# Optimization experiments

Hardware: AMD Instinct MI355X
Metric: run time of the kernel (lower is better)

## Reference

```python
import jax, jax.numpy as jnp
import numpy as np

B, N, D, H, DG = 1, 1024, 512, 8, 64
DK = D // H
EPS = 1e-5


def _layer_norm(x, g, b):
    m = jnp.mean(x, axis=-1, keepdims=True)
    v = jnp.var(x, axis=-1, keepdims=True)
    return (x - m) / jnp.sqrt(v + EPS) * g + b


def _box_rel_embedding(box):
    # box: (B, N, 4) = x_min, y_min, x_max, y_max
    x_min, y_min, x_max, y_max = [box[..., i] for i in range(4)]  # each (B, N)
    cx = (x_min + x_max) * 0.5
    cy = (y_min + y_max) * 0.5
    w = x_max - x_min + 1.0
    h = y_max - y_min + 1.0
    dx = jnp.log(jnp.clip(jnp.abs((cx[:, :, None] - cx[:, None, :]) / w[:, :, None]), 0.001))
    dy = jnp.log(jnp.clip(jnp.abs((cy[:, :, None] - cy[:, None, :]) / h[:, :, None]), 0.001))
    dw = jnp.log(w[:, :, None] / w[:, None, :])
    dh = jnp.log(h[:, :, None] / h[:, None, :])
    pos = jnp.stack([dx, dy, dw, dh], axis=-1)  # (B, N, N, 4)
    dim_mat = 1.0 / jnp.power(1000.0, jnp.arange(DG // 8, dtype=jnp.float32) / (DG // 8))  # (8,)
    mul = (100.0 * pos[..., None] * dim_mat).reshape(pos.shape[0], pos.shape[1], pos.shape[2], -1)  # (B,N,N,32)
    return jnp.concatenate([jnp.sin(mul), jnp.cos(mul)], axis=-1)  # (B, N, N, 64)


def _split_heads(x, W, b):
    # torch permute(2,0,1,3).view(-1, len, d_k): head-major flattening
    return (x @ W.T + b).reshape(B, N, H, DK).transpose(2, 0, 1, 3).reshape(H * B, N, DK)


def _forward(input_query, input_key, input_value, input_box,
             Wq, bq, Wk, bk, Wv, bv, Wo, bo, WG_w, WG_b,
             ln0_g, ln0_b, ln_g, ln_b):
    residual = input_query
    emb = _box_rel_embedding(input_box)  # (B, N, N, 64)
    # per-head linear (64 -> 1) then relu: (B, H, N, N)
    w_g = jax.nn.relu(jnp.einsum('bijg,hg->bhij', emb, WG_w) + WG_b[None, :, None, None])
    q = _split_heads(input_query, Wq, bq)  # (H*B, N, DK)
    k = _split_heads(input_key, Wk, bk)
    v = _split_heads(input_value, Wv, bv)
    scores = jnp.einsum('xnd,xmd->xnm', q, k) / np.sqrt(DK).astype(np.float32)  # (H*B, N, N)
    # original adds (B,H,N,N) to (H*B,N,N): only valid for B==1
    w_mn = jax.nn.softmax(jnp.log(jnp.clip(w_g.reshape(H * B, N, N), 1e-6)) + scores, axis=-1)
    x = jnp.einsum('xnm,xmd->xnd', w_mn, v)  # (H*B, N, DK)
    # faithful to original: transpose(1,2) then view(nbatches, -1, h*d_k)
    x = x.transpose(0, 2, 1).reshape(B, -1, H * DK)  # (B, N, D)
    out0 = _layer_norm(x + residual, ln0_g, ln0_b)
    out = out0 @ Wo.T + bo  # dropout = identity (eval mode)
    return _layer_norm(out + out0, ln_g, ln_b)


def setup_inputs() -> dict:
    key = jax.random.key(0)
    ks = jax.random.split(key, 12)
    inp = {}
    inp['input_query'] = jax.random.normal(ks[0], (B, N, D), dtype=jnp.float32)
    inp['input_key'] = jax.random.normal(ks[1], (B, N, D), dtype=jnp.float32)
    inp['input_value'] = jax.random.normal(ks[2], (B, N, D), dtype=jnp.float32)
    mins = jax.random.uniform(ks[3], (B, N, 2), dtype=jnp.float32) * 500.0
    sizes = jax.random.uniform(ks[4], (B, N, 2), dtype=jnp.float32) * 99.0 + 1.0
    inp['input_box'] = jnp.concatenate([mins, mins + sizes], axis=-1)  # valid boxes
    s = 0.02
    inp['Wq'] = jax.random.normal(ks[5], (D, D), dtype=jnp.float32) * s
    inp['bq'] = jnp.zeros((D,), dtype=jnp.float32)
    inp['Wk'] = jax.random.normal(ks[6], (D, D), dtype=jnp.float32) * s
    inp['bk'] = jnp.zeros((D,), dtype=jnp.float32)
    inp['Wv'] = jax.random.normal(ks[7], (D, D), dtype=jnp.float32) * s
    inp['bv'] = jnp.zeros((D,), dtype=jnp.float32)
    inp['Wo'] = jax.random.normal(ks[8], (D, D), dtype=jnp.float32) * s
    inp['bo'] = jnp.zeros((D,), dtype=jnp.float32)
    inp['WG_w'] = jax.random.normal(ks[9], (H, DG), dtype=jnp.float32) * 0.1
    inp['WG_b'] = jax.random.normal(ks[10], (H,), dtype=jnp.float32) * 0.1
    inp['ln0_g'] = jnp.ones((D,), dtype=jnp.float32)
    inp['ln0_b'] = jnp.zeros((D,), dtype=jnp.float32)
    inp['ln_g'] = jnp.ones((D,), dtype=jnp.float32)
    inp['ln_b'] = jnp.zeros((D,), dtype=jnp.float32)
    return inp


def reference(input_query, input_key, input_value, input_box,
              Wq, bq, Wk, bk, Wv, bv, Wo, bo, WG_w, WG_b,
              ln0_g, ln0_b, ln_g, ln_b):
    return _forward(input_query, input_key, input_value, input_box,
                    Wq, bq, Wk, bk, Wv, bv, Wo, bo, WG_w, WG_b,
                    ln0_g, ln0_b, ln_g, ln_b)
```

## Files before the change

kernel.cpp:

```cpp
#include <hip/hip_runtime.h>
#include <cstddef>

#define NTOK 1024
#define DMODEL 512
#define NHEAD 8
#define DKH 64
#define NSPLIT 4
#define JQ 256

typedef __attribute__((ext_vector_type(4))) float f32x4;
typedef __attribute__((ext_vector_type(8))) __bf16 bf16x8;
typedef __attribute__((ext_vector_type(4))) __bf16 bf16x4;
typedef __attribute__((ext_vector_type(4))) unsigned short u16x4;
typedef __attribute__((ext_vector_type(8))) unsigned short u16x8;
typedef __attribute__((ext_vector_type(4))) _Float16 f16x4;
typedef unsigned short ushort_t;

__device__ __forceinline__ float wave_sum_f(float v){
  #pragma unroll
  for (int m=1; m<64; m<<=1) v += __shfl_xor(v, m, 64);
  return v;
}
__device__ __forceinline__ unsigned short f2bf(float f){
  __bf16 b = (__bf16)f;
  return __builtin_bit_cast(unsigned short, b);
}
__device__ __forceinline__ float bf2f(unsigned short u){
  return (float)__builtin_bit_cast(__bf16, u);
}

__device__ __forceinline__ float fract_hw(float x){
  float r; asm("v_fract_f32 %0, %1" : "=v"(r) : "v"(x)); return r;
}
__device__ __forceinline__ float sin_rev(float rev){
  float f = fract_hw(rev);
  float s; asm("v_sin_f32 %0, %1" : "=v"(s) : "v"(f)); return s;
}
__device__ __forceinline__ float cos_rev(float rev){
  float f = fract_hw(rev);
  float c; asm("v_cos_f32 %0, %1" : "=v"(c) : "v"(f)); return c;
}
__device__ __forceinline__ float log_hw(float x){
  float l; asm("v_log_f32 %0, %1" : "=v"(l) : "v"(x));
  return 0.69314718056f * l;
}
__device__ __forceinline__ float exp_hw(float x){
  float y = x * 1.44269504f;
  float e; asm("v_exp_f32 %0, %1" : "=v"(e) : "v"(y));
  return e;
}

__global__ __launch_bounds__(256) void k_front2(
    const float* __restrict__ box, const float* __restrict__ WGw, const float* __restrict__ WGb,
    _Float16* __restrict__ wg16,
    const float* __restrict__ inq, const float* __restrict__ ink, const float* __restrict__ inv,
    const float* __restrict__ Wq, const float* __restrict__ Wk, const float* __restrict__ Wv,
    const float* __restrict__ Wo,
    const float* __restrict__ bq, const float* __restrict__ bk, const float* __restrict__ bv,
    ushort_t* __restrict__ Qb, ushort_t* __restrict__ Kb, ushort_t* __restrict__ Vt,
    ushort_t* __restrict__ Wob){
  __shared__ __align__(16) char smem[17408];
  const int t = threadIdx.x;
  const int lane = t & 63, w = t >> 6, li = lane & 15, g = lane >> 4;
  if (blockIdx.x >= 1408){
    int off = ((blockIdx.x - 1408)*256 + t)*8;
    float4 a = *(const float4*)(Wo + off);
    float4 b4 = *(const float4*)(Wo + off + 4);
    u16x4 o0, o1;
    o0[0]=f2bf(a.x); o0[1]=f2bf(a.y); o0[2]=f2bf(a.z); o0[3]=f2bf(a.w);
    o1[0]=f2bf(b4.x); o1[1]=f2bf(b4.y); o1[2]=f2bf(b4.z); o1[3]=f2bf(b4.w);
    *(u16x4*)(Wob + off) = o0;
    *(u16x4*)(Wob + off + 4) = o1;
    return;
  }
  if (blockIdx.x >= 1024){
    const int u = blockIdx.x - 1024;
    const int z = u >> 7;
    const int rem = u & 127;
    const int m0 = (rem >> 3)*64;
    const int n0 = (rem & 7)*64;
    const float* A = z==0 ? inq : z==1 ? ink : inv;
    const float* W = z==0 ? Wq : z==1 ? Wk : Wv;
    const float* bias = z==0 ? bq : z==1 ? bk : bv;
    ushort_t* Al = (ushort_t*)smem;
    ushort_t* Wl = (ushort_t*)(smem + 8704);
    const int row = t >> 2, kq = (t & 3)*16;
    const int mrb = (w >> 1)*32;
    const int nrb = (w & 1)*32;
    f32x4 acc[2][2] = {};
    for (int k0 = 0; k0 < DMODEL; k0 += 64){
      {
        const float* ap = A + (size_t)(m0+row)*DMODEL + k0 + kq;
        const float* wp = W + (size_t)(n0+row)*DMODEL + k0 + kq;
        #pragma unroll
        for (int q=0; q<4; q++){
          float4 av = *(const float4*)(ap + q*4);
          float4 wv = *(const float4*)(wp + q*4);
          u16x4 pa, pw;
          pa[0]=f2bf(av.x); pa[1]=f2bf(av.y); pa[2]=f2bf(av.z); pa[3]=f2bf(av.w);
          pw[0]=f2bf(wv.x); pw[1]=f2bf(wv.y); pw[2]=f2bf(wv.z); pw[3]=f2bf(wv.w);
          *(u16x4*)(Al + row*68 + kq + q*4) = pa;
          *(u16x4*)(Wl + row*68 + kq + q*4) = pw;
        }
      }
      __syncthreads();
      #pragma unroll
      for (int kc=0; kc<64; kc+=32){
        const ushort_t* arl = Al + (mrb + li)*68 + kc + g*8;
        const ushort_t* wrl = Wl + (nrb + li)*68 + kc + g*8;
        bf16x8 af0 = *(const bf16x8*)(arl);
        bf16x8 af1 = *(const bf16x8*)(arl + 16*68);
        bf16x8 wf0 = *(const bf16x8*)(wrl);
        bf16x8 wf1 = *(const bf16x8*)(wrl + 16*68);
        if (z < 2){
          acc[0][0] = __builtin_amdgcn_mfma_f32_16x16x32_bf16(wf0, af0, acc[0][0], 0,0,0);
          acc[0][1] = __builtin_amdgcn_mfma_f32_16x16x32_bf16(wf0, af1, acc[0][1], 0,0,0);
          acc[1][0] = __builtin_amdgcn_mfma_f32_16x16x32_bf16(wf1, af0, acc[1][0], 0,0,0);
          acc[1][1] = __builtin_amdgcn_mfma_f32_16x16x32_bf16(wf1, af1, acc[1][1], 0,0,0);
        } else {
          acc[0][0] = __builtin_amdgcn_mfma_f32_16x16x32_bf16(af0, wf0, acc[0][0], 0,0,0);
          acc[0][1] = __builtin_amdgcn_mfma_f32_16x16x32_bf16(af0, wf1, acc[0][1], 0,0,0);
          acc[1][0] = __builtin_amdgcn_mfma_f32_16x16x32_bf16(af1, wf0, acc[1][0], 0,0,0);
          acc[1][1] = __builtin_amdgcn_mfma_f32_16x16x32_bf16(af1, wf1, acc[1][1], 0,0,0);
        }
      }
      __syncthreads();
    }
    if (z < 2){
      ushort_t* C = z ? Kb : Qb;
      #pragma unroll
      for (int nf=0; nf<2; nf++){
        int n = n0 + nrb + nf*16 + g*4;
        float4 b4 = *(const float4*)(bias + n);
        const float* bp = (const float*)&b4;
        #pragma unroll
        for (int mf=0; mf<2; mf++){
          int m = m0 + mrb + mf*16 + li;
          u16x4 o;
          #pragma unroll
          for (int r=0; r<4; r++) o[r] = f2bf(acc[nf][mf][r] + bp[r]);
          *(u16x4*)(C + (size_t)m*DMODEL + n) = o;
        }
      }
    } else {
      #pragma unroll
      for (int mf=0; mf<2; mf++){
        int m = m0 + mrb + mf*16 + g*4;
        #pragma unroll
        for (int nf=0; nf<2; nf++){
          int n = n0 + nrb + nf*16 + li;
          float bn = bias[n];
          u16x4 o;
          #pragma unroll
          for (int r=0; r<4; r++) o[r] = f2bf(acc[mf][nf][r] + bn);
          *(u16x4*)(Vt + (((size_t)(n>>6))<<16) + ((size_t)(n&63)<<10) + m) = o;
        }
      }
    }
    return;
  }
  float* arr = (float*)smem;
  #pragma unroll
  for (int u2=0; u2<4; u2++){
    int idx = u2*256 + t;
    float4 b4 = *(const float4*)(box + idx*4);
    arr[idx]        = (b4.x + b4.z)*0.5f;
    arr[1024+idx]   = (b4.y + b4.w)*0.5f;
    arr[2048+idx]   = log_hw(b4.z - b4.x + 1.0f);
    arr[3072+idx]   = log_hw(b4.w - b4.y + 1.0f);
  }
  const int i = blockIdx.x;
  float4 bi = *(const float4*)(box + i*4);
  float wi = bi.z - bi.x + 1.0f, hi = bi.w - bi.y + 1.0f;
  float Pi = (g==0) ? (bi.x+bi.z)*0.5f : (g==1) ? (bi.y+bi.w)*0.5f
           : (g==2) ? log_hw(wi) : log_hw(hi);
  float Ri = (g==0) ? 1.0f/wi : (g==1) ? 1.0f/hi : 1.0f;
  const bool doLog = (g < 2);
  bf16x8 wfs = {}, wfc = {};
  float wgb_li = 0.0f;
  if (li < 8){
    #pragma unroll
    for (int e=0; e<8; e++){
      wfs[e] = (__bf16)WGw[li*64 + g*8 + e];
      wfc[e] = (__bf16)WGw[li*64 + 32 + g*8 + e];
    }
    wgb_li = WGb[li];
  }
  __syncthreads();
  const float* parr = arr + g*1024;
  const float DMrev[8] = {15.9154943f, 6.7115094f, 2.8302196f, 1.1934938f,
                          0.5032921f, 0.2122365f, 0.08949941f, 0.0377416f};
  const int jbeg = w*256;
  for (int it=0; it<16; ++it){
    int j = jbeg + it*16 + li;
    float diff = (Pi - parr[j])*Ri;
    float lg = log_hw(fmaxf(fabsf(diff), 1e-3f));
    float dv = doLog ? lg : diff;
    bf16x8 afs, afc;
    #pragma unroll
    for (int e=0; e<8; e++){
      float rev = dv * DMrev[e];
      afs[e] = (__bf16)sin_rev(rev);
      afc[e] = (__bf16)cos_rev(rev);
    }
    f32x4 acc = (f32x4){0.f,0.f,0.f,0.f};
    acc = __builtin_amdgcn_mfma_f32_16x16x32_bf16(afs, wfs, acc, 0,0,0);
    acc = __builtin_amdgcn_mfma_f32_16x16x32_bf16(afc, wfc, acc, 0,0,0);
    if (li < 8){
      f16x4 o;
      #pragma unroll
      for (int r=0; r<4; r++)
        o[r] = (_Float16)fmaxf(acc[r] + wgb_li, 6.103515625e-05f);
      *(f16x4*)(wg16 + (((size_t)li<<20) + ((size_t)i<<10) + jbeg + it*16 + g*4)) = o;
    }
  }
}

__global__ __launch_bounds__(512) void k_attn3(const ushort_t* __restrict__ Qb,
     const ushort_t* __restrict__ Kb, const ushort_t* __restrict__ Vt,
     const _Float16* __restrict__ wg, ushort_t* __restrict__ Xpt, float* __restrict__ rsp){
  __shared__ ushort_t Ks[256*68];
  __shared__ ushort_t Vs[64*264];
  const int t = threadIdx.x;
  const int itg = blockIdx.x, h = blockIdx.y, sp = blockIdx.z;
  const int jbeg = sp*JQ;
  {
    const int r = t >> 3, c = (t & 7)*8;
    #pragma unroll
    for (int p=0; p<4; p++){
      u16x8 kv = *(const u16x8*)(Kb + (size_t)(jbeg + p*64 + r)*DMODEL + h*DKH + c);
      *(u16x8*)(Ks + (p*64 + r)*68 + c) = kv;
      u16x8 vv = *(const u16x8*)(Vt + ((size_t)h<<16) + (size_t)r*NTOK + jbeg + p*64 + c);
      *(u16x8*)(Vs + r*264 + p*64 + c) = vv;
    }
  }
  const int lane = t & 63, w = t >> 6;
  const int i0 = (itg*8 + w)*16;
  const int li = lane & 15, g = lane >> 4;
  const ushort_t* qp = Qb + (size_t)(i0+li)*DMODEL + h*DKH + g*8;
  bf16x8 qf0 = *(const bf16x8*)(qp);
  bf16x8 qf1 = *(const bf16x8*)(qp + 32);
  const _Float16* gbase = wg + ((size_t)h<<20) + ((size_t)(i0+li)<<10) + jbeg + g*4;
  f32x4 xacc[4];
  #pragma unroll
  for (int mf=0; mf<4; mf++) xacc[mf] = (f32x4){0.f,0.f,0.f,0.f};
  float rsum = 0.f;
  __syncthreads();
  #pragma unroll
  for (int jj = 0; jj < JQ; jj += 32){
    const ushort_t* kp = Ks + (jj + li)*68 + g*8;
    bf16x8 a00 = *(const bf16x8*)(kp);
    bf16x8 a01 = *(const bf16x8*)(kp + 32);
    bf16x8 a10 = *(const bf16x8*)(kp + 16*68);
    bf16x8 a11 = *(const bf16x8*)(kp + 16*68 + 32);
    f32x4 s0 = (f32x4){0.f,0.f,0.f,0.f};
    f32x4 s1 = (f32x4){0.f,0.f,0.f,0.f};
    s0 = __builtin_amdgcn_mfma_f32_16x16x32_bf16(a00, qf0, s0, 0,0,0);
    s0 = __builtin_amdgcn_mfma_f32_16x16x32_bf16(a01, qf1, s0, 0,0,0);
    s1 = __builtin_amdgcn_mfma_f32_16x16x32_bf16(a10, qf0, s1, 0,0,0);
    s1 = __builtin_amdgcn_mfma_f32_16x16x32_bf16(a11, qf1, s1, 0,0,0);
    f16x4 g0 = *(const f16x4*)(gbase + jj);
    f16x4 g1 = *(const f16x4*)(gbase + jj + 16);
    float p[8];
    #pragma unroll
    for (int r=0; r<4; r++){ p[r]   = (float)g0[r] * exp_hw(s0[r]*0.125f); rsum += p[r]; }
    #pragma unroll
    for (int r=0; r<4; r++){ p[4+r] = (float)g1[r] * exp_hw(s1[r]*0.125f); rsum += p[4+r]; }
    bf16x8 pb;
    pb[0]=(__bf16)p[0]; pb[1]=(__bf16)p[1]; pb[2]=(__bf16)p[2]; pb[3]=(__bf16)p[3];
    pb[4]=(__bf16)p[4]; pb[5]=(__bf16)p[5]; pb[6]=(__bf16)p[6]; pb[7]=(__bf16)p[7];
    #pragma unroll
    for (int mf=0; mf<4; mf++){
      const ushort_t* vp = Vs + (size_t)(li + mf*16)*264 + jj + g*4;
      bf16x4 lo = *(const bf16x4*)(vp);
      bf16x4 hi = *(const bf16x4*)(vp + 16);
      bf16x8 vf = __builtin_shufflevector(lo, hi, 0,1,2,3,4,5,6,7);
      xacc[mf] = __builtin_amdgcn_mfma_f32_16x16x32_bf16(vf, pb, xacc[mf], 0,0,0);
    }
  }
  rsum += __shfl_xor(rsum, 16, 64);
  rsum += __shfl_xor(rsum, 32, 64);
  if (lane < 16) rsp[((size_t)sp*NHEAD + h)*NTOK + i0 + li] = rsum;
  __syncthreads();
  float* xw = (float*)Ks + w*(16*68);
  #pragma unroll
  for (int mf=0; mf<4; mf++)
    *(f32x4*)&xw[li*68 + mf*16 + g*4] = xacc[mf];
  __builtin_amdgcn_s_waitcnt(0);
  float xv[16];
  #pragma unroll
  for (int r=0; r<16; r++) xv[r] = xw[r*68 + lane];
  u16x8 o0, o1;
  #pragma unroll
  for (int r=0; r<8; r++){ o0[r] = f2bf(xv[r]); o1[r] = f2bf(xv[8+r]); }
  ushort_t* xp = Xpt + (((size_t)sp*NHEAD + h)*DKH + lane)*NTOK + i0;
  *(u16x8*)(xp)     = o0;
  *(u16x8*)(xp + 8) = o1;
}

__global__ __launch_bounds__(512) void k_back2(
    const ushort_t* __restrict__ Xpt, const float* __restrict__ rsp,
    const float* __restrict__ inq,
    const float* __restrict__ ln0g, const float* __restrict__ ln0b,
    const ushort_t* __restrict__ Wob, const float* __restrict__ bo,
    const float* __restrict__ lng, const float* __restrict__ lnb,
    float* __restrict__ out){
  __shared__ ushort_t Ab[8][520];
  __shared__ float    Y[8][516];
  __shared__ float    red[8][8][2];
  const int t = threadIdx.x, lane = t & 63, w = t >> 6;
  const int li = lane & 15, g = lane >> 4;
  const int m0 = blockIdx.x*8;
  {
    const int n = m0 + w;
    const int h = n >> 7, dk = (n >> 1) & 63, mo = (n & 1)*512;
    float x[8];
    float sum = 0.f, sq = 0.f;
    #pragma unroll
    for (int c=0; c<8; c++){
      int d = c*64 + lane;
      int i = mo + d;
      float sv = 0.f, rv = 0.f;
      #pragma unroll
      for (int sp=0; sp<NSPLIT; sp++){
        sv += bf2f(Xpt[(((size_t)sp*NHEAD + h)*DKH + dk)*NTOK + i]);
        rv += rsp[((size_t)sp*NHEAD + h)*NTOK + i];
      }
      x[c] = sv/rv + inq[(size_t)n*DMODEL + d];
      sum += x[c]; sq += x[c]*x[c];
    }
    sum = wave_sum_f(sum);
    sq  = wave_sum_f(sq);
    float mean = sum * (1.0f/512.0f);
    float var = sq * (1.0f/512.0f) - mean*mean;
    float rs = rsqrtf(var + 1e-5f);
    #pragma unroll
    for (int c=0; c<8; c++){
      int d = c*64 + lane;
      float y = (x[c]-mean)*rs*ln0g[d] + ln0b[d];
      Y[w][d] = y;
      Ab[w][d] = f2bf(y);
    }
  }
  __syncthreads();
  const int n0 = w*64;
  const ushort_t* ar = &Ab[li & 7][g*8];
  const ushort_t* wr = Wob + (size_t)(n0+li)*DMODEL + g*8;
  f32x4 acc[4] = {};
  #pragma unroll
  for (int k0=0; k0<DMODEL; k0+=64){
    bf16x8 afa = *(const bf16x8*)(ar + k0);
    bf16x8 afb = *(const bf16x8*)(ar + k0 + 32);
    #pragma unroll
    for (int nf=0; nf<4; nf++){
      const ushort_t* wp = wr + (size_t)nf*16*DMODEL + k0;
      bf16x8 wfa = *(const bf16x8*)(wp);
      bf16x8 wfb = *(const bf16x8*)(wp + 32);
      acc[nf] = __builtin_amdgcn_mfma_f32_16x16x32_bf16(wfa, afa, acc[nf], 0,0,0);
      acc[nf] = __builtin_amdgcn_mfma_f32_16x16x32_bf16(wfb, afb, acc[nf], 0,0,0);
    }
  }
  float s = 0.f, qq = 0.f;
  f32x4 v[4];
  #pragma unroll
  for (int nf=0; nf<4; nf++){
    int n = n0 + nf*16 + g*4;
    f32x4 b4 = *(const f32x4*)(bo + n);
    #pragma unroll
    for (int r=0; r<4; r++){
      float x = acc[nf][r] + b4[r] + Y[li & 7][n + r];
      v[nf][r] = x; s += x; qq += x*x;
    }
  }
  s  += __shfl_xor(s, 16, 64);  s  += __shfl_xor(s, 32, 64);
  qq += __shfl_xor(qq, 16, 64); qq += __shfl_xor(qq, 32, 64);
  if (g == 0 && li < 8){ red[w][li][0] = s; red[w][li][1] = qq; }
  __syncthreads();
  float S = 0.f, Q = 0.f;
  #pragma unroll
  for (int u=0; u<8; u++){ S += red[u][li & 7][0]; Q += red[u][li & 7][1]; }
  float mean = S * (1.0f/512.0f);
  float var = Q * (1.0f/512.0f) - mean*mean;
  float rs = rsqrtf(var + 1e-5f);
  if (li < 8){
    const int m = m0 + li;
    #pragma unroll
    for (int nf=0; nf<4; nf++){
      int n = n0 + nf*16 + g*4;
      f32x4 g4 = *(const f32x4*)(lng + n);
      f32x4 be = *(const f32x4*)(lnb + n);
      f32x4 o;
      #pragma unroll
      for (int r=0; r<4; r++) o[r] = (v[nf][r]-mean)*rs*g4[r] + be[r];
      *(f32x4*)(out + (size_t)m*DMODEL + n) = o;
    }
  }
}

extern "C" void kernel_launch(void* const* d_in, const int* in_sizes, int n_in,
                              void* d_out, int out_size, void* d_ws, size_t ws_size,
                              hipStream_t stream){
  (void)in_sizes; (void)n_in; (void)out_size; (void)ws_size;
  const float* in_q = (const float*)d_in[0];
  const float* in_k = (const float*)d_in[1];
  const float* in_v = (const float*)d_in[2];
  const float* box  = (const float*)d_in[3];
  const float* Wq   = (const float*)d_in[4];
  const float* bq   = (const float*)d_in[5];
  const float* Wk   = (const float*)d_in[6];
  const float* bk   = (const float*)d_in[7];
  const float* Wv   = (const float*)d_in[8];
  const float* bv   = (const float*)d_in[9];
  const float* Wo   = (const float*)d_in[10];
  const float* bo   = (const float*)d_in[11];
  const float* WGw  = (const float*)d_in[12];
  const float* WGb  = (const float*)d_in[13];
  const float* ln0g = (const float*)d_in[14];
  const float* ln0b = (const float*)d_in[15];
  const float* lng  = (const float*)d_in[16];
  const float* lnb  = (const float*)d_in[17];

  float* ws = (float*)d_ws;
  ushort_t* Wob  = (ushort_t*)(ws + 0);
  ushort_t* Qb   = (ushort_t*)(ws + 131072);
  ushort_t* Kb   = (ushort_t*)(ws + 393216);
  ushort_t* Vt   = (ushort_t*)(ws + 655360);
  _Float16* wg16 = (_Float16*)(ws + 917504);
  ushort_t* Xpt  = (ushort_t*)(ws + 5111808);
  float*    rsp  = ws + 6160384;
  float*    out  = (float*)d_out;

  k_front2<<<dim3(1536), dim3(256), 0, stream>>>(box, WGw, WGb, wg16,
            in_q, in_k, in_v, Wq, Wk, Wv, Wo, bq, bk, bv, Qb, Kb, Vt, Wob);
  k_attn3<<<dim3(8,8,4), dim3(512), 0, stream>>>(Qb, Kb, Vt, wg16, Xpt, rsp);
  k_back2<<<dim3(128), dim3(512), 0, stream>>>(Xpt, rsp, in_q, ln0g, ln0b,
            Wob, bo, lng, lnb, out);
}
```

Measured before the change: 66.73 us.

## Merge attention and output-projection kernels using a global atomic counter barrier

Fuses the attention kernel and the back-end LayerNorm/output-projection kernel into one launch of 384 blocks. The first 256 blocks do attention and signal completion through an agent-scope atomic counter, and the remaining 128 blocks spin on that counter before running the projection and norms. The aim is to remove one kernel launch and its inter-kernel gap, at the cost of a memset launch, spin-waiting blocks that hold CU resources, and a deadlock risk if the waiting blocks get scheduled before the attention blocks can all run.

```diff
diff --git a/kernel.cpp b/kernel.cpp
--- a/kernel.cpp
+++ b/kernel.cpp
@@ -48,6 +48,19 @@
   float y = x * 1.44269504f;
   float e; asm("v_exp_f32 %0, %1" : "=v"(e) : "v"(y));
   return e;
+}
+
+__device__ __forceinline__ void mark_done(unsigned* c){
+  __syncthreads();
+  if (threadIdx.x == 0)
+    __hip_atomic_fetch_add(c, 1u, __ATOMIC_RELEASE, __HIP_MEMORY_SCOPE_AGENT);
+}
+__device__ __forceinline__ void wait_for(unsigned* c, unsigned target){
+  if (threadIdx.x == 0){
+    while (__hip_atomic_load(c, __ATOMIC_ACQUIRE, __HIP_MEMORY_SCOPE_AGENT) < target)
+      __builtin_amdgcn_s_sleep(8);
+  }
+  __syncthreads();
 }
 
 __global__ __launch_bounds__(256) void k_front2(
@@ -216,183 +229,186 @@
   }
 }
 
-__global__ __launch_bounds__(512) void k_attn3(const ushort_t* __restrict__ Qb,
+__global__ __launch_bounds__(512) void k_ab(const ushort_t* __restrict__ Qb,
      const ushort_t* __restrict__ Kb, const ushort_t* __restrict__ Vt,
-     const _Float16* __restrict__ wg, ushort_t* __restrict__ Xpt, float* __restrict__ rsp){
-  __shared__ ushort_t Ks[256*68];
-  __shared__ ushort_t Vs[64*264];
+     const _Float16* __restrict__ wg, ushort_t* __restrict__ Xpt, float* __restrict__ rsp,
+     const float* __restrict__ inq,
+     const float* __restrict__ ln0g, const float* __restrict__ ln0b,
+     const ushort_t* __restrict__ Wob, const float* __restrict__ bo,
+     const float* __restrict__ lng, const float* __restrict__ lnb,
+     float* __restrict__ out, unsigned* bar){
+  __shared__ __align__(16) char smem[68608];
   const int t = threadIdx.x;
-  const int itg = blockIdx.x, h = blockIdx.y, sp = blockIdx.z;
-  const int jbeg = sp*JQ;
+  const int b = blockIdx.x;
+  const int lane = t & 63, w = t >> 6, li = lane & 15, g = lane >> 4;
+
+  if (b < 256){
+    ushort_t* Ks = (ushort_t*)smem;
+    ushort_t* Vs = (ushort_t*)(smem + 34816);
+    const int itg = b & 7, h = (b >> 3) & 7, sp = b >> 6;
+    const int jbeg = sp*JQ;
+    {
+      const int r = t >> 3, c = (t & 7)*8;
+      #pragma unroll
+      for (int p=0; p<4; p++){
+        u16x8 kv = *(const u16x8*)(Kb + (size_t)(jbeg + p*64 + r)*DMODEL + h*DKH + c);
+        *(u16x8*)(Ks + (p*64 + r)*68 + c) = kv;
+        u16x8 vv = *(const u16x8*)(Vt + ((size_t)h<<16) + (size_t)r*NTOK + jbeg + p*64 + c);
+        *(u16x8*)(Vs + r*264 + p*64 + c) = vv;
+      }
+    }
+    const int i0 = (itg*8 + w)*16;
+    const ushort_t* qp = Qb + (size_t)(i0+li)*DMODEL + h*DKH + g*8;
+    bf16x8 qf0 = *(const bf16x8*)(qp);
+    bf16x8 qf1 = *(const bf16x8*)(qp + 32);
+    const _Float16* gbase = wg + ((size_t)h<<20) + ((size_t)(i0+li)<<10) + jbeg + g*4;
+    f32x4 xacc[4];
+    #pragma unroll
+    for (int mf=0; mf<4; mf++) xacc[mf] = (f32x4){0.f,0.f,0.f,0.f};
+    float rsum = 0.f;
+    __syncthreads();
+    #pragma unroll
+    for (int jj = 0; jj < JQ; jj += 32){
+      const ushort_t* kp = Ks + (jj + li)*68 + g*8;
+      bf16x8 a00 = *(const bf16x8*)(kp);
+      bf16x8 a01 = *(const bf16x8*)(kp + 32);
+      bf16x8 a10 = *(const bf16x8*)(kp + 16*68);
+      bf16x8 a11 = *(const bf16x8*)(kp + 16*68 + 32);
+      f32x4 s0 = (f32x4){0.f,0.f,0.f,0.f};
+      f32x4 s1 = (f32x4){0.f,0.f,0.f,0.f};
+      s0 = __builtin_amdgcn_mfma_f32_16x16x32_bf16(a00, qf0, s0, 0,0,0);
+      s0 = __builtin_amdgcn_mfma_f32_16x16x32_bf16(a01, qf1, s0, 0,0,0);
+      s1 = __builtin_amdgcn_mfma_f32_16x16x32_bf16(a10, qf0, s1, 0,0,0);
+      s1 = __builtin_amdgcn_mfma_f32_16x16x32_bf16(a11, qf1, s1, 0,0,0);
+      f16x4 g0 = *(const f16x4*)(gbase + jj);
+      f16x4 g1 = *(const f16x4*)(gbase + jj + 16);
+      float p[8];
+      #pragma unroll
+      for (int r=0; r<4; r++){ p[r]   = (float)g0[r] * exp_hw(s0[r]*0.125f); rsum += p[r]; }
+      #pragma unroll
+      for (int r=0; r<4; r++){ p[4+r] = (float)g1[r] * exp_hw(s1[r]*0.125f); rsum += p[4+r]; }
+      bf16x8 pb;
+      pb[0]=(__bf16)p[0]; pb[1]=(__bf16)p[1]; pb[2]=(__bf16)p[2]; pb[3]=(__bf16)p[3];
+      pb[4]=(__bf16)p[4]; pb[5]=(__bf16)p[5]; pb[6]=(__bf16)p[6]; pb[7]=(__bf16)p[7];
+      #pragma unroll
+      for (int mf=0; mf<4; mf++){
+        const ushort_t* vp = Vs + (size_t)(li + mf*16)*264 + jj + g*4;
+        bf16x4 lo = *(const bf16x4*)(vp);
+        bf16x4 hi = *(const bf16x4*)(vp + 16);
+        bf16x8 vf = __builtin_shufflevector(lo, hi, 0,1,2,3,4,5,6,7);
+        xacc[mf] = __builtin_amdgcn_mfma_f32_16x16x32_bf16(vf, pb, xacc[mf], 0,0,0);
+      }
+    }
+    rsum += __shfl_xor(rsum, 16, 64);
+    rsum += __shfl_xor(rsum, 32, 64);
+    if (lane < 16) rsp[((size_t)sp*NHEAD + h)*NTOK + i0 + li] = rsum;
+    __syncthreads();
+    float* xw = (float*)Ks + w*(16*68);
+    #pragma unroll
+    for (int mf=0; mf<4; mf++)
+      *(f32x4*)&xw[li*68 + mf*16 + g*4] = xacc[mf];
+    __builtin_amdgcn_s_waitcnt(0);
+    float xv[16];
+    #pragma unroll
+    for (int r=0; r<16; r++) xv[r] = xw[r*68 + lane];
+    u16x8 o0, o1;
+    #pragma unroll
+    for (int r=0; r<8; r++){ o0[r] = f2bf(xv[r]); o1[r] = f2bf(xv[8+r]); }
+    ushort_t* xp = Xpt + (((size_t)sp*NHEAD + h)*DKH + lane)*NTOK + i0;
+    *(u16x8*)(xp)     = o0;
+    *(u16x8*)(xp + 8) = o1;
+    mark_done(bar);
+    return;
+  }
   {
-    const int r = t >> 3, c = (t & 7)*8;
-    #pragma unroll
-    for (int p=0; p<4; p++){
-      u16x8 kv = *(const u16x8*)(Kb + (size_t)(jbeg + p*64 + r)*DMODEL + h*DKH + c);
-      *(u16x8*)(Ks + (p*64 + r)*68 + c) = kv;
-      u16x8 vv = *(const u16x8*)(Vt + ((size_t)h<<16) + (size_t)r*NTOK + jbeg + p*64 + c);
-      *(u16x8*)(Vs + r*264 + p*64 + c) = vv;
-    }
-  }
-  const int lane = t & 63, w = t >> 6;
-  const int i0 = (itg*8 + w)*16;
-  const int li = lane & 15, g = lane >> 4;
-  const ushort_t* qp = Qb + (size_t)(i0+li)*DMODEL + h*DKH + g*8;
-  bf16x8 qf0 = *(const bf16x8*)(qp);
-  bf16x8 qf1 = *(const bf16x8*)(qp + 32);
-  const _Float16* gbase = wg + ((size_t)h<<20) + ((size_t)(i0+li)<<10) + jbeg + g*4;
-  f32x4 xacc[4];
-  #pragma unroll
-  for (int mf=0; mf<4; mf++) xacc[mf] = (f32x4){0.f,0.f,0.f,0.f};
-  float rsum = 0.f;
-  __syncthreads();
-  #pragma unroll
-  for (int jj = 0; jj < JQ; jj += 32){
-    const ushort_t* kp = Ks + (jj + li)*68 + g*8;
-    bf16x8 a00 = *(const bf16x8*)(kp);
-    bf16x8 a01 = *(const bf16x8*)(kp + 32);
-    bf16x8 a10 = *(const bf16x8*)(kp + 16*68);
-    bf16x8 a11 = *(const bf16x8*)(kp + 16*68 + 32);
-    f32x4 s0 = (f32x4){0.f,0.f,0.f,0.f};
-    f32x4 s1 = (f32x4){0.f,0.f,0.f,0.f};
-    s0 = __builtin_amdgcn_mfma_f32_16x16x32_bf16(a00, qf0, s0, 0,0,0);
-    s0 = __builtin_amdgcn_mfma_f32_16x16x32_bf16(a01, qf1, s0, 0,0,0);
-    s1 = __builtin_amdgcn_mfma_f32_16x16x32_bf16(a10, qf0, s1, 0,0,0);
-    s1 = __builtin_amdgcn_mfma_f32_16x16x32_bf16(a11, qf1, s1, 0,0,0);
-    f16x4 g0 = *(const f16x4*)(gbase + jj);
-    f16x4 g1 = *(const f16x4*)(gbase + jj + 16);
-    float p[8];
-    #pragma unroll
-    for (int r=0; r<4; r++){ p[r]   = (float)g0[r] * exp_hw(s0[r]*0.125f); rsum += p[r]; }
-    #pragma unroll
-    for (int r=0; r<4; r++){ p[4+r] = (float)g1[r] * exp_hw(s1[r]*0.125f); rsum += p[4+r]; }
-    bf16x8 pb;
-    pb[0]=(__bf16)p[0]; pb[1]=(__bf16)p[1]; pb[2]=(__bf16)p[2]; pb[3]=(__bf16)p[3];
-    pb[4]=(__bf16)p[4]; pb[5]=(__bf16)p[5]; pb[6]=(__bf16)p[6]; pb[7]=(__bf16)p[7];
-    #pragma unroll
-    for (int mf=0; mf<4; mf++){
-      const ushort_t* vp = Vs + (size_t)(li + mf*16)*264 + jj + g*4;
-      bf16x4 lo = *(const bf16x4*)(vp);
-      bf16x4 hi = *(const bf16x4*)(vp + 16);
-      bf16x8 vf = __builtin_shufflevector(lo, hi, 0,1,2,3,4,5,6,7);
-      xacc[mf] = __builtin_amdgcn_mfma_f32_16x16x32_bf16(vf, pb, xacc[mf], 0,0,0);
-    }
-  }
-  rsum += __shfl_xor(rsum, 16, 64);
-  rsum += __shfl_xor(rsum, 32, 64);
-  if (lane < 16) rsp[((size_t)sp*NHEAD + h)*NTOK + i0 + li] = rsum;
-  __syncthreads();
-  float* xw = (float*)Ks + w*(16*68);
-  #pragma unroll
-  for (int mf=0; mf<4; mf++)
-    *(f32x4*)&xw[li*68 + mf*16 + g*4] = xacc[mf];
-  __builtin_amdgcn_s_waitcnt(0);
-  float xv[16];
-  #pragma unroll
-  for (int r=0; r<16; r++) xv[r] = xw[r*68 + lane];
-  u16x8 o0, o1;
-  #pragma unroll
-  for (int r=0; r<8; r++){ o0[r] = f2bf(xv[r]); o1[r] = f2bf(xv[8+r]); }
-  ushort_t* xp = Xpt + (((size_t)sp*NHEAD + h)*DKH + lane)*NTOK + i0;
-  *(u16x8*)(xp)     = o0;
-  *(u16x8*)(xp + 8) = o1;
-}
-
-__global__ __launch_bounds__(512) void k_back2(
-    const ushort_t* __restrict__ Xpt, const float* __restrict__ rsp,
-    const float* __restrict__ inq,
-    const float* __restrict__ ln0g, const float* __restrict__ ln0b,
-    const ushort_t* __restrict__ Wob, const float* __restrict__ bo,
-    const float* __restrict__ lng, const float* __restrict__ lnb,
-    float* __restrict__ out){
-  __shared__ ushort_t Ab[8][520];
-  __shared__ float    Y[8][516];
-  __shared__ float    red[8][8][2];
-  const int t = threadIdx.x, lane = t & 63, w = t >> 6;
-  const int li = lane & 15, g = lane >> 4;
-  const int m0 = blockIdx.x*8;
-  {
-    const int n = m0 + w;
-    const int h = n >> 7, dk = (n >> 1) & 63, mo = (n & 1)*512;
-    float x[8];
-    float sum = 0.f, sq = 0.f;
-    #pragma unroll
-    for (int c=0; c<8; c++){
-      int d = c*64 + lane;
-      int i = mo + d;
-      float sv = 0.f, rv = 0.f;
-      #pragma unroll
-      for (int sp=0; sp<NSPLIT; sp++){
-        sv += bf2f(Xpt[(((size_t)sp*NHEAD + h)*DKH + dk)*NTOK + i]);
-        rv += rsp[((size_t)sp*NHEAD + h)*NTOK + i];
-      }
-      x[c] = sv/rv + inq[(size_t)n*DMODEL + d];
-      sum += x[c]; sq += x[c]*x[c];
-    }
-    sum = wave_sum_f(sum);
-    sq  = wave_sum_f(sq);
-    float mean = sum * (1.0f/512.0f);
-    float var = sq * (1.0f/512.0f) - mean*mean;
-    float rs = rsqrtf(var + 1e-5f);
-    #pragma unroll
-    for (int c=0; c<8; c++){
-      int d = c*64 + lane;
-      float y = (x[c]-mean)*rs*ln0g[d] + ln0b[d];
-      Y[w][d] = y;
-      Ab[w][d] = f2bf(y);
-    }
-  }
-  __syncthreads();
-  const int n0 = w*64;
-  const ushort_t* ar = &Ab[li & 7][g*8];
-  const ushort_t* wr = Wob + (size_t)(n0+li)*DMODEL + g*8;
-  f32x4 acc[4] = {};
-  #pragma unroll
-  for (int k0=0; k0<DMODEL; k0+=64){
-    bf16x8 afa = *(const bf16x8*)(ar + k0);
-    bf16x8 afb = *(const bf16x8*)(ar + k0 + 32);
-    #pragma unroll
-    for (int nf=0; nf<4; nf++){
-      const ushort_t* wp = wr + (size_t)nf*16*DMODEL + k0;
-      bf16x8 wfa = *(const bf16x8*)(wp);
-      bf16x8 wfb = *(const bf16x8*)(wp + 32);
-      acc[nf] = __builtin_amdgcn_mfma_f32_16x16x32_bf16(wfa, afa, acc[nf], 0,0,0);
-      acc[nf] = __builtin_amdgcn_mfma_f32_16x16x32_bf16(wfb, afb, acc[nf], 0,0,0);
-    }
-  }
-  float s = 0.f, qq = 0.f;
-  f32x4 v[4];
-  #pragma unroll
-  for (int nf=0; nf<4; nf++){
-    int n = n0 + nf*16 + g*4;
-    f32x4 b4 = *(const f32x4*)(bo + n);
-    #pragma unroll
-    for (int r=0; r<4; r++){
-      float x = acc[nf][r] + b4[r] + Y[li & 7][n + r];
-      v[nf][r] = x; s += x; qq += x*x;
-    }
-  }
-  s  += __shfl_xor(s, 16, 64);  s  += __shfl_xor(s, 32, 64);
-  qq += __shfl_xor(qq, 16, 64); qq += __shfl_xor(qq, 32, 64);
-  if (g == 0 && li < 8){ red[w][li][0] = s; red[w][li][1] = qq; }
-  __syncthreads();
-  float S = 0.f, Q = 0.f;
-  #pragma unroll
-  for (int u=0; u<8; u++){ S += red[u][li & 7][0]; Q += red[u][li & 7][1]; }
-  float mean = S * (1.0f/512.0f);
-  float var = Q * (1.0f/512.0f) - mean*mean;
-  float rs = rsqrtf(var + 1e-5f);
-  if (li < 8){
-    const int m = m0 + li;
+    wait_for(bar, 256u);
+    ushort_t* Ab = (ushort_t*)smem;
+    float*    Y  = (float*)(smem + 8320);
+    float*    red= (float*)(smem + 24832);
+    const int m0 = (b - 256)*8;
+    {
+      const int n = m0 + w;
+      const int h = n >> 7, dk = (n >> 1) & 63, mo = (n & 1)*512;
+      float x[8];
+      float sum = 0.f, sq = 0.f;
+      #pragma unroll
+      for (int c=0; c<8; c++){
+        int d = c*64 + lane;
+        int i = mo + d;
+        float sv = 0.f, rv = 0.f;
+        #pragma unroll
+        for (int sp=0; sp<NSPLIT; sp++){
+          sv += bf2f(Xpt[(((size_t)sp*NHEAD + h)*DKH + dk)*NTOK + i]);
+          rv += rsp[((size_t)sp*NHEAD + h)*NTOK + i];
+        }
+        x[c] = sv/rv + inq[(size_t)n*DMODEL + d];
+        sum += x[c]; sq += x[c]*x[c];
+      }
+      sum = wave_sum_f(sum);
+      sq  = wave_sum_f(sq);
+      float mean = sum * (1.0f/512.0f);
+      float var = sq * (1.0f/512.0f) - mean*mean;
+      float rs = rsqrtf(var + 1e-5f);
+      #pragma unroll
+      for (int c=0; c<8; c++){
+        int d = c*64 + lane;
+        float y = (x[c]-mean)*rs*ln0g[d] + ln0b[d];
+        Y[w*516 + d] = y;
+        Ab[w*520 + d] = f2bf(y);
+      }
+    }
+    __syncthreads();
+    const int n0 = w*64;
+    const ushort_t* ar = Ab + (li & 7)*520 + g*8;
+    const ushort_t* wr = Wob + (size_t)(n0+li)*DMODEL + g*8;
+    f32x4 acc[4] = {};
+    #pragma unroll
+    for (int k0=0; k0<DMODEL; k0+=64){
+      bf16x8 afa = *(const bf16x8*)(ar + k0);
+      bf16x8 afb = *(const bf16x8*)(ar + k0 + 32);
+      #pragma unroll
+      for (int nf=0; nf<4; nf++){
+        const ushort_t* wp = wr + (size_t)nf*16*DMODEL + k0;
+        bf16x8 wfa = *(const bf16x8*)(wp);
+        bf16x8 wfb = *(const bf16x8*)(wp + 32);
+        acc[nf] = __builtin_amdgcn_mfma_f32_16x16x32_bf16(wfa, afa, acc[nf], 0,0,0);
+        acc[nf] = __builtin_amdgcn_mfma_f32_16x16x32_bf16(wfb, afb, acc[nf], 0,0,0);
+      }
+    }
+    float s = 0.f, qq = 0.f;
+    f32x4 v[4];
     #pragma unroll
     for (int nf=0; nf<4; nf++){
       int n = n0 + nf*16 + g*4;
-      f32x4 g4 = *(const f32x4*)(lng + n);
-      f32x4 be = *(const f32x4*)(lnb + n);
-      f32x4 o;
-      #pragma unroll
-      for (int r=0; r<4; r++) o[r] = (v[nf][r]-mean)*rs*g4[r] + be[r];
-      *(f32x4*)(out + (size_t)m*DMODEL + n) = o;
+      f32x4 b4 = *(const f32x4*)(bo + n);
+      #pragma unroll
+      for (int r=0; r<4; r++){
+        float x = acc[nf][r] + b4[r] + Y[(li & 7)*516 + n + r];
+        v[nf][r] = x; s += x; qq += x*x;
+      }
+    }
+    s  += __shfl_xor(s, 16, 64);  s  += __shfl_xor(s, 32, 64);
+    qq += __shfl_xor(qq, 16, 64); qq += __shfl_xor(qq, 32, 64);
+    if (g == 0 && li < 8){ red[(w*8 + li)*2] = s; red[(w*8 + li)*2 + 1] = qq; }
+    __syncthreads();
+    float S = 0.f, Q = 0.f;
+    #pragma unroll
+    for (int u=0; u<8; u++){ S += red[(u*8 + (li & 7))*2]; Q += red[(u*8 + (li & 7))*2 + 1]; }
+    float mean = S * (1.0f/512.0f);
+    float var = Q * (1.0f/512.0f) - mean*mean;
+    float rs = rsqrtf(var + 1e-5f);
+    if (li < 8){
+      const int m = m0 + li;
+      #pragma unroll
+      for (int nf=0; nf<4; nf++){
+        int n = n0 + nf*16 + g*4;
+        f32x4 g4 = *(const f32x4*)(lng + n);
+        f32x4 be = *(const f32x4*)(lnb + n);
+        f32x4 o;
+        #pragma unroll
+        for (int r=0; r<4; r++) o[r] = (v[nf][r]-mean)*rs*g4[r] + be[r];
+        *(f32x4*)(out + (size_t)m*DMODEL + n) = o;
+      }
     }
   }
 }
@@ -428,11 +444,12 @@
   _Float16* wg16 = (_Float16*)(ws + 917504);
   ushort_t* Xpt  = (ushort_t*)(ws + 5111808);
   float*    rsp  = ws + 6160384;
+  unsigned* bar  = (unsigned*)(ws + 6193152);
   float*    out  = (float*)d_out;
 
+  hipMemsetAsync(bar, 0, 8, stream);
   k_front2<<<dim3(1536), dim3(256), 0, stream>>>(box, WGw, WGb, wg16,
             in_q, in_k, in_v, Wq, Wk, Wv, Wo, bq, bk, bv, Qb, Kb, Vt, Wob);
-  k_attn3<<<dim3(8,8,4), dim3(512), 0, stream>>>(Qb, Kb, Vt, wg16, Xpt, rsp);
-  k_back2<<<dim3(128), dim3(512), 0, stream>>>(Xpt, rsp, in_q, ln0g, ln0b,
-            Wob, bo, lng, lnb, out);
-}
+  k_ab<<<dim3(384), dim3(512), 0, stream>>>(Qb, Kb, Vt, wg16, Xpt, rsp,
+            in_q, ln0g, ln0b, Wob, bo, lng, lnb, out, bar);
+}
```

Measured after the change: 94.22 us. +41.2%, slower.
